# Performance work log

Measured on AMD Instinct MI355X. Metric: run time of the kernel, lower is better.

Reference implementation:

```python
import jax, jax.numpy as jnp
import numpy as np
import math

EMBED = 1024
N_HEAD = 16
T_LEN = 2048
BATCH = 2
MLP_MULT = 4
EPS = 1e-5


def setup_inputs() -> dict:
    key = jax.random.key(0)
    ks = jax.random.split(key, 12)
    d = EMBED
    h = MLP_MULT * d
    s = 0.02
    return {
        "x": jax.random.normal(ks[0], (BATCH, T_LEN, d), dtype=jnp.float32),
        "ln1_scale": jnp.ones((d,), jnp.float32),
        "ln1_shift": jnp.zeros((d,), jnp.float32),
        "w_qkv": jax.random.normal(ks[1], (d, 3 * d), jnp.float32) * s,
        "b_qkv": jnp.zeros((3 * d,), jnp.float32),
        "ln2_scale": jnp.ones((d,), jnp.float32),
        "ln2_shift": jnp.zeros((d,), jnp.float32),
        "w_fc": jax.random.normal(ks[2], (d, h), jnp.float32) * s,
        "b_fc": jnp.zeros((h,), jnp.float32),
        "w_proj": jax.random.normal(ks[3], (h, d), jnp.float32) * s,
        "b_proj": jnp.zeros((d,), jnp.float32),
    }


def _layer_norm(x, scale, shift):
    mu = jnp.mean(x, axis=-1, keepdims=True)
    var = jnp.var(x, axis=-1, keepdims=True)
    return (x - mu) * jax.lax.rsqrt(var + EPS) * scale + shift


def _attention(h, w_qkv, b_qkv):
    B, T, C = h.shape
    hd = C // N_HEAD
    qkv = h @ w_qkv + b_qkv  # [B,T,3C]
    q, k, v = jnp.split(qkv, 3, axis=-1)
    q = q.reshape(B, T, N_HEAD, hd)
    k = k.reshape(B, T, N_HEAD, hd)
    v = v.reshape(B, T, N_HEAD, hd)
    scores = jnp.einsum("bthd,bshd->bhts", q, k) * (1.0 / math.sqrt(hd))
    causal = jnp.tril(jnp.ones((T, T), dtype=bool))
    scores = jnp.where(causal[None, None], scores, -jnp.inf)
    probs = jax.nn.softmax(scores, axis=-1)
    y = jnp.einsum("bhts,bshd->bthd", probs, v)
    return y.reshape(B, T, C)


def reference(x, ln1_scale, ln1_shift, w_qkv, b_qkv, ln2_scale, ln2_shift,
              w_fc, b_fc, w_proj, b_proj):
    x = x + _attention(_layer_norm(x, ln1_scale, ln1_shift), w_qkv, b_qkv)
    h = _layer_norm(x, ln2_scale, ln2_shift)
    # note: module names it 'gelu' but it's nn.ReLU()
    h = jax.nn.relu(h @ w_fc + b_fc) @ w_proj + b_proj
    return x + h
```

## Files before the change

kernel.cpp:

```cpp
#include <hip/hip_runtime.h>
#include <hip/hip_bf16.h>


typedef __bf16  bf16x8  __attribute__((ext_vector_type(8)));
typedef __bf16  bf16x4  __attribute__((ext_vector_type(4)));
typedef float   floatx4 __attribute__((ext_vector_type(4)));

#define T_LEN 2048
#define EMB   1024
#define NH    16
#define HD    64
#define HID   4096

#define GLOBAL_LOAD_LDS16(gp, lp) \
    __builtin_amdgcn_global_load_lds( \
        (const __attribute__((address_space(1))) void*)(gp), \
        (__attribute__((address_space(3))) void*)(lp), 16, 0, 0)

__global__ void transpose_cast(const float* __restrict__ in,
                               __bf16* __restrict__ out, int R, int C) {
    __shared__ float tile[32][33];
    int bc = blockIdx.x * 32;
    int br = blockIdx.y * 32;
    int tx = threadIdx.x;
    int ty = threadIdx.y;
    for (int i = 0; i < 32; i += 8) {
        tile[ty + i][tx] = in[(size_t)(br + ty + i) * C + bc + tx];
    }
    __syncthreads();
    for (int i = 0; i < 32; i += 8) {
        int c = bc + ty + i, r = br + tx;
        out[(size_t)c * R + r] = (__bf16)tile[tx][ty + i];
    }
}

__global__ __launch_bounds__(256)
void ln_kernel(const float* __restrict__ in, const float* __restrict__ sc,
               const float* __restrict__ sh, __bf16* __restrict__ out) {
    int row = blockIdx.x;
    const float* p = in + (size_t)row * EMB;
    int tid = threadIdx.x;
    int lane = tid & 63, wave = tid >> 6;
    float v[4];
    float s = 0.f, s2 = 0.f;
    for (int j = 0; j < 4; j++) {
        v[j] = p[tid + j * 256];
        s += v[j]; s2 += v[j] * v[j];
    }
    for (int m = 1; m < 64; m <<= 1) {
        s  += __shfl_xor(s, m);
        s2 += __shfl_xor(s2, m);
    }
    __shared__ float ssum[4], ssum2[4];
    if (lane == 0) { ssum[wave] = s; ssum2[wave] = s2; }
    __syncthreads();
    float tot  = ssum[0] + ssum[1] + ssum[2] + ssum[3];
    float tot2 = ssum2[0] + ssum2[1] + ssum2[2] + ssum2[3];
    float mean = tot * (1.f / EMB);
    float var  = tot2 * (1.f / EMB) - mean * mean;
    float rstd = rsqrtf(var + 1e-5f);
    for (int j = 0; j < 4; j++) {
        int c = tid + j * 256;
        out[(size_t)row * EMB + c] = (__bf16)((v[j] - mean) * rstd * sc[c] + sh[c]);
    }
}

__global__ __launch_bounds__(512)
void gemm256(const __bf16* __restrict__ A, const __bf16* __restrict__ Bt,
             const float* __restrict__ bias, const float* __restrict__ res,
             float* __restrict__ outF, __bf16* __restrict__ outB,
             int M, int N, int lda, int KL, int relu, int gx, int gz) {
    __shared__ __align__(16) __bf16 sA[2][256][64];
    __shared__ __align__(16) __bf16 sB[2][256][64];
    const int BUFE = 256 * 64;
    int tid  = threadIdx.x;
    int lane = tid & 63, wave = tid >> 6;
    int quad = lane >> 4, l16 = lane & 15;

    int i  = blockIdx.x;
    int c  = i & 7, m = i >> 3;
    int bx = m % gx;
    int p  = (m / gx) * 8 + c;
    int by = p / gz;
    int bz = p - by * gz;

    int bm = by * 256, bn = bx * 256;
    size_t k0 = (size_t)bz * KL;
    int wm = (wave >> 2) * 128, wn = (wave & 3) * 64;

    floatx4 acc[8][4] = {};

    int srow  = tid >> 3;
    int sslot = (tid & 7) ^ (srow & 7);
    const __bf16* gA = A  + (size_t)(bm + srow) * lda + k0 + sslot * 8;
    const __bf16* gB = Bt + (size_t)(bn + srow) * lda + k0 + sslot * 8;
    __bf16* lA = &sA[0][0][0] + wave * 512;
    __bf16* lB = &sB[0][0][0] + wave * 512;
    const size_t rstep = (size_t)64 * lda;

#define STAGE256(nb, ko) do { \
    GLOBAL_LOAD_LDS16(gA + (ko),             lA + (nb) * BUFE); \
    GLOBAL_LOAD_LDS16(gB + (ko),             lB + (nb) * BUFE); \
    GLOBAL_LOAD_LDS16(gA + (ko) + rstep,     lA + (nb) * BUFE + 4096); \
    GLOBAL_LOAD_LDS16(gB + (ko) + rstep,     lB + (nb) * BUFE + 4096); \
    GLOBAL_LOAD_LDS16(gA + (ko) + 2 * rstep, lA + (nb) * BUFE + 8192); \
    GLOBAL_LOAD_LDS16(gB + (ko) + 2 * rstep, lB + (nb) * BUFE + 8192); \
    GLOBAL_LOAD_LDS16(gA + (ko) + 3 * rstep, lA + (nb) * BUFE + 12288); \
    GLOBAL_LOAD_LDS16(gB + (ko) + 3 * rstep, lB + (nb) * BUFE + 12288); \
} while (0)

    STAGE256(0, (size_t)0);

    int xs0  = ((quad) ^ (l16 & 7)) * 8;
    int xs1  = ((4 + quad) ^ (l16 & 7)) * 8;
    int aoff = (wm + l16) * 64;
    int boff = (wn + l16) * 64;

    const int nt = KL / 64;
    for (int t = 0; t < nt; ++t) {
        const int cur = t & 1;
        __builtin_amdgcn_s_barrier();
        asm volatile("" ::: "memory");
        if (t + 1 < nt) {
            STAGE256(cur ^ 1, (size_t)(t + 1) * 64);
            asm volatile("s_waitcnt vmcnt(8)" ::: "memory");
        } else {
            asm volatile("s_waitcnt vmcnt(0)" ::: "memory");
        }
        __builtin_amdgcn_s_barrier();
        asm volatile("" ::: "memory");
        __builtin_amdgcn_sched_barrier(0);

        const __bf16* sAc = &sA[0][0][0] + cur * BUFE;
        const __bf16* sBc = &sB[0][0][0] + cur * BUFE;

        bf16x8 a0[4][2], a1[4][2], b0[2][2], b1[2][2];

        #pragma unroll
        for (int mi = 0; mi < 4; ++mi) {
            a0[mi][0] = *(const bf16x8*)(sAc + aoff + mi * 1024 + xs0);
            a0[mi][1] = *(const bf16x8*)(sAc + aoff + mi * 1024 + xs1);
        }
        #pragma unroll
        for (int nj = 0; nj < 2; ++nj) {
            b0[nj][0] = *(const bf16x8*)(sBc + boff + nj * 1024 + xs0);
            b0[nj][1] = *(const bf16x8*)(sBc + boff + nj * 1024 + xs1);
        }
        __builtin_amdgcn_s_setprio(1);
        #pragma unroll
        for (int ks = 0; ks < 2; ++ks)
            #pragma unroll
            for (int mi = 0; mi < 4; ++mi)
                #pragma unroll
                for (int nj = 0; nj < 2; ++nj)
                    acc[mi][nj] = __builtin_amdgcn_mfma_f32_16x16x32_bf16(
                        a0[mi][ks], b0[nj][ks], acc[mi][nj], 0, 0, 0);
        __builtin_amdgcn_s_setprio(0);

        #pragma unroll
        for (int nj = 0; nj < 2; ++nj) {
            b1[nj][0] = *(const bf16x8*)(sBc + boff + (2 + nj) * 1024 + xs0);
            b1[nj][1] = *(const bf16x8*)(sBc + boff + (2 + nj) * 1024 + xs1);
        }
        __builtin_amdgcn_s_setprio(1);
        #pragma unroll
        for (int ks = 0; ks < 2; ++ks)
            #pragma unroll
            for (int mi = 0; mi < 4; ++mi)
                #pragma unroll
                for (int nj = 0; nj < 2; ++nj)
                    acc[mi][2 + nj] = __builtin_amdgcn_mfma_f32_16x16x32_bf16(
                        a0[mi][ks], b1[nj][ks], acc[mi][2 + nj], 0, 0, 0);
        __builtin_amdgcn_s_setprio(0);

        #pragma unroll
        for (int mi = 0; mi < 4; ++mi) {
            a1[mi][0] = *(const bf16x8*)(sAc + aoff + (4 + mi) * 1024 + xs0);
            a1[mi][1] = *(const bf16x8*)(sAc + aoff + (4 + mi) * 1024 + xs1);
        }
        __builtin_amdgcn_s_setprio(1);
        #pragma unroll
        for (int ks = 0; ks < 2; ++ks)
            #pragma unroll
            for (int mi = 0; mi < 4; ++mi)
                #pragma unroll
                for (int nj = 0; nj < 2; ++nj)
                    acc[4 + mi][2 + nj] = __builtin_amdgcn_mfma_f32_16x16x32_bf16(
                        a1[mi][ks], b1[nj][ks], acc[4 + mi][2 + nj], 0, 0, 0);
        __builtin_amdgcn_s_setprio(0);

        __builtin_amdgcn_s_setprio(1);
        #pragma unroll
        for (int ks = 0; ks < 2; ++ks)
            #pragma unroll
            for (int mi = 0; mi < 4; ++mi)
                #pragma unroll
                for (int nj = 0; nj < 2; ++nj)
                    acc[4 + mi][nj] = __builtin_amdgcn_mfma_f32_16x16x32_bf16(
                        a1[mi][ks], b0[nj][ks], acc[4 + mi][nj], 0, 0, 0);
        __builtin_amdgcn_s_setprio(0);
    }
#undef STAGE256

    if (bias) {
        #pragma unroll
        for (int mi = 0; mi < 8; ++mi) {
            int row0 = bm + wm + mi * 16 + quad * 4;
            #pragma unroll
            for (int nj = 0; nj < 4; ++nj) {
                int col = bn + wn + nj * 16 + l16;
                float bv = bias[col];
                #pragma unroll
                for (int r = 0; r < 4; ++r) {
                    size_t idx = (size_t)(row0 + r) * N + col;
                    float cc = acc[mi][nj][r] + bv;
                    if (relu) cc = fmaxf(cc, 0.f);
                    if (res)  cc += res[idx];
                    if (outF) outF[idx] = cc;
                    if (outB) outB[idx] = (__bf16)cc;
                }
            }
        }
    } else {
        __bf16* po = outB + (size_t)bz * M * N;
        #pragma unroll
        for (int mi = 0; mi < 8; ++mi) {
            int row0 = bm + wm + mi * 16 + quad * 4;
            #pragma unroll
            for (int nj = 0; nj < 4; ++nj) {
                int col = bn + wn + nj * 16 + l16;
                #pragma unroll
                for (int r = 0; r < 4; ++r)
                    po[(size_t)(row0 + r) * N + col] = (__bf16)acc[mi][nj][r];
            }
        }
    }
}

__global__ __launch_bounds__(256)
void reduce_proj(const __bf16* __restrict__ pbuf, const float* __restrict__ x2,
                 const float* __restrict__ bias, float* __restrict__ out) {
    const size_t MN = (size_t)4096 * 1024;
    size_t i = (size_t)blockIdx.x * 256 + threadIdx.x;
    float4 r = ((const float4*)x2)[i];
    float4 bb = ((const float4*)bias)[i & 255];
    float acc0 = r.x + bb.x, acc1 = r.y + bb.y;
    float acc2 = r.z + bb.z, acc3 = r.w + bb.w;
    for (int k = 0; k < 4; k++) {
        bf16x4 pv = *(const bf16x4*)&pbuf[k * MN + i * 4];
        acc0 += (float)pv[0]; acc1 += (float)pv[1];
        acc2 += (float)pv[2]; acc3 += (float)pv[3];
    }
    float4 o = {acc0, acc1, acc2, acc3};
    ((float4*)out)[i] = o;
}

__global__ __launch_bounds__(256)
void gemm_bt_n64(const __bf16* __restrict__ A, const __bf16* __restrict__ Bt,
                 const float* __restrict__ bias, const float* __restrict__ res,
                 float* __restrict__ outF, __bf16* __restrict__ outB,
                 int M, int N, int K, int relu) {
    __shared__ __align__(16) __bf16 sA[128][40];
    __shared__ __align__(16) __bf16 sB[64][40];
    int tid  = threadIdx.x;
    int lane = tid & 63, wave = tid >> 6;
    int quad = lane >> 4, l16 = lane & 15;
    int bm = blockIdx.y * 128, bn = blockIdx.x * 64;
    int wm = (wave & 1) * 64, wn = (wave >> 1) * 32;
    floatx4 acc[4][2] = {};

    int srow = tid >> 2;
    int scol = (tid & 3) * 8;
    const __bf16* gA = &A[(size_t)(bm + srow) * K + scol];
    const __bf16* gB = &Bt[(size_t)(bn + srow) * K + scol];

    uint4 ra0 = *(const uint4*)gA;
    uint4 ra1 = *(const uint4*)(gA + (size_t)64 * K);
    uint4 rb0 = *(const uint4*)gB;

    for (int kk = 0; kk < K; kk += 32) {
        __syncthreads();
        *(uint4*)&sA[srow][scol]      = ra0;
        *(uint4*)&sA[srow + 64][scol] = ra1;
        *(uint4*)&sB[srow][scol]      = rb0;
        __syncthreads();
        {
            int kn = (kk + 32 < K) ? kk + 32 : kk;
            ra0 = *(const uint4*)(gA + kn);
            ra1 = *(const uint4*)(gA + kn + (size_t)64 * K);
            rb0 = *(const uint4*)(gB + kn);
        }
        bf16x8 af[4], bfr[2];
        for (int i = 0; i < 4; i++)
            af[i] = *(const bf16x8*)&sA[wm + i * 16 + l16][quad * 8];
        for (int j = 0; j < 2; j++)
            bfr[j] = *(const bf16x8*)&sB[wn + j * 16 + l16][quad * 8];
        for (int i = 0; i < 4; i++)
            for (int j = 0; j < 2; j++)
                acc[i][j] = __builtin_amdgcn_mfma_f32_16x16x32_bf16(
                    af[i], bfr[j], acc[i][j], 0, 0, 0);
    }

    for (int i = 0; i < 4; i++) {
        int row0 = bm + wm + i * 16 + quad * 4;
        for (int j = 0; j < 2; j++) {
            int col = bn + wn + j * 16 + l16;
            float bv = bias[col];
            for (int r = 0; r < 4; r++) {
                size_t idx = (size_t)(row0 + r) * N + col;
                float c = acc[i][j][r] + bv;
                if (relu) c = fmaxf(c, 0.f);
                if (res)  c += res[idx];
                if (outF) outF[idx] = c;
                if (outB) outB[idx] = (__bf16)c;
            }
        }
    }
}

__global__ __launch_bounds__(512)
void attn_kernel(const __bf16* __restrict__ qkv, const float* __restrict__ x,
                 float* __restrict__ x2) {
    __shared__ __align__(16) __bf16 sK[2][64][72];
    __shared__ __align__(16) __bf16 sVt[2][64][72];
    __shared__ __align__(16) __bf16 sP[8][16][72];
    const int tid  = threadIdx.x;
    const int lane = tid & 63, wave = tid >> 6;
    const int quad = lane >> 4, l16 = lane & 15;

    int i = blockIdx.x;
    int c = i & 7, m = i >> 3;
    const int bh   = (m & 3) * 8 + c;
    const int qt_h = 31 - (m >> 2);
    const int h    = bh & (NH - 1);
    const int b    = bh >> 4;
    const size_t rowbase = (size_t)b * T_LEN;

    const int g  = wave >> 2;
    const int wg = wave & 3;
    const int qt = g ? (31 - qt_h) : qt_h;
    const int qrow = qt * 64 + wg * 16;
    const int dt   = qt;

    const float kQScale = 0.125f * 1.44269504088896f;
    bf16x8 ones;
    for (int j = 0; j < 8; j++) ones[j] = (__bf16)1.0f;

    const int key0 = tid >> 3, m8 = tid & 7;
    const __bf16* kp0 = qkv + (rowbase + key0) * 3072 + h * HD + m8 * 8 + 1024;
    const int pc0 = ((key0 >> 3) ^ m8) * 8 + (key0 & 7);

    bf16x8 qf[2];
    for (int ks = 0; ks < 2; ks++) {
        bf16x8 raw = *(const bf16x8*)&qkv[(rowbase + qrow + l16) * 3072
                                          + h * HD + ks * 32 + quad * 8];
        for (int j = 0; j < 8; j++)
            qf[ks][j] = (__bf16)((float)raw[j] * kQScale);
    }

    floatx4 o[4] = {}, ol = {};

    const int ntiles = qt_h + 1;
    const size_t TSTEP = (size_t)64 * 3072;

    uint4 kr0 = *(const uint4*)kp0;
    uint4 vr0 = *(const uint4*)(kp0 + 1024);
    {
        *(uint4*)&sK[0][key0][m8 * 8] = kr0;
        bf16x8 v0 = *(bf16x8*)&vr0;
        for (int j = 0; j < 8; j++) sVt[0][m8 * 8 + j][pc0] = v0[j];
    }
    kr0 = *(const uint4*)(kp0 + TSTEP);
    vr0 = *(const uint4*)(kp0 + TSTEP + 1024);
    __syncthreads();

    for (int kt = 0; kt < ntiles; kt++) {
        const int cur = kt & 1, nxt = cur ^ 1;
        if (kt + 1 < ntiles) {
            *(uint4*)&sK[nxt][key0][m8 * 8] = kr0;
            bf16x8 v0 = *(bf16x8*)&vr0;
            for (int j = 0; j < 8; j++) sVt[nxt][m8 * 8 + j][pc0] = v0[j];
            size_t offn = (size_t)((kt + 2 < ntiles) ? kt + 2 : kt + 1) * TSTEP;
            kr0 = *(const uint4*)(kp0 + offn);
            vr0 = *(const uint4*)(kp0 + offn + 1024);
        }

        if (kt <= dt) {
            floatx4 s_acc[4] = {};
            for (int jt = 0; jt < 4; jt++)
                for (int ks = 0; ks < 2; ks++) {
                    bf16x8 kf = *(const bf16x8*)&sK[cur][jt * 16 + l16]
                                                  [ks * 32 + quad * 8];
                    s_acc[jt] = __builtin_amdgcn_mfma_f32_16x16x32_bf16(
                        qf[ks], kf, s_acc[jt], 0, 0, 0);
                }

            if (kt == dt) {
                const int tq0 = qrow + quad * 4;
                const int k0 = kt * 64;
                for (int jt = 0; jt < 4; jt++) {
                    int key = k0 + jt * 16 + l16;
                    for (int r = 0; r < 4; r++) {
                        float sv = (key <= tq0 + r) ? s_acc[jt][r] : -1e30f;
                        float pv = __builtin_amdgcn_exp2f(fminf(sv, 30.f));
                        sP[wave][quad * 4 + r][jt * 16 + l16] = (__bf16)pv;
                    }
                }
            } else {
                for (int jt = 0; jt < 4; jt++)
                    for (int r = 0; r < 4; r++) {
                        float pv = __builtin_amdgcn_exp2f(fminf(s_acc[jt][r], 30.f));
                        sP[wave][quad * 4 + r][jt * 16 + l16] = (__bf16)pv;
                    }
            }

            for (int kp = 0; kp < 2; kp++) {
                bf16x8 pf = *(const bf16x8*)&sP[wave][l16][kp * 32 + quad * 8];
                ol = __builtin_amdgcn_mfma_f32_16x16x32_bf16(pf, ones, ol, 0, 0, 0);
                for (int jt2 = 0; jt2 < 4; jt2++) {
                    int d = jt2 * 16 + l16;
                    int pg = (kp * 4 + quad) ^ (d >> 3);
                    bf16x8 vf = *(const bf16x8*)&sVt[cur][d][pg * 8];
                    o[jt2] = __builtin_amdgcn_mfma_f32_16x16x32_bf16(
                        pf, vf, o[jt2], 0, 0, 0);
                }
            }
        }
        __syncthreads();
    }

    float inv[4];
    for (int r = 0; r < 4; r++) inv[r] = __builtin_amdgcn_rcpf(ol[r]);
    for (int jt2 = 0; jt2 < 4; jt2++) {
        for (int r = 0; r < 4; r++) {
            int tq  = qrow + quad * 4 + r;
            int col = h * HD + jt2 * 16 + l16;
            size_t gi = (rowbase + tq) * EMB + col;
            x2[gi] = x[gi] + o[jt2][r] * inv[r];
        }
    }
}

extern "C" void kernel_launch(void* const* d_in, const int* in_sizes, int n_in,
                              void* d_out, int out_size, void* d_ws, size_t ws_size,
                              hipStream_t stream) {
    const float* x      = (const float*)d_in[0];
    const float* ln1_s  = (const float*)d_in[1];
    const float* ln1_b  = (const float*)d_in[2];
    const float* w_qkv  = (const float*)d_in[3];
    const float* b_qkv  = (const float*)d_in[4];
    const float* ln2_s  = (const float*)d_in[5];
    const float* ln2_b  = (const float*)d_in[6];
    const float* w_fc   = (const float*)d_in[7];
    const float* b_fc   = (const float*)d_in[8];
    const float* w_proj = (const float*)d_in[9];
    const float* b_proj = (const float*)d_in[10];
    float* out = (float*)d_out;

    const int M = 2 * T_LEN;
    char* ws = (char*)d_ws;
    size_t off = 0;
    auto alloc = [&](size_t bytes) {
        void* p = ws + off; off += (bytes + 255) & ~(size_t)255; return p;
    };
    __bf16* wpj_t  = (__bf16*)alloc((size_t)1024 * 4096 * 2);
    float*  x2     = (float*) alloc((size_t)M * 1024 * 4);
    __bf16* hfc    = (__bf16*)alloc((size_t)M * 4096 * 2);
    size_t mark = off;
    __bf16* wqkv_t = (__bf16*)alloc((size_t)3072 * 1024 * 2);
    __bf16* wfc_t  = (__bf16*)alloc((size_t)4096 * 1024 * 2);
    __bf16* h1     = (__bf16*)alloc((size_t)M * 1024 * 2);
    __bf16* h2     = (__bf16*)alloc((size_t)M * 1024 * 2);
    __bf16* qkvb   = (__bf16*)alloc((size_t)M * 3072 * 2);
    __bf16* pbuf = (__bf16*)(ws + mark);
    size_t need = mark + (size_t)4 * M * 1024 * 2;
    bool can_split = ws_size >= need;

    dim3 tb(32, 8);
    transpose_cast<<<dim3(3072 / 32, 1024 / 32), tb, 0, stream>>>(w_qkv, wqkv_t, 1024, 3072);
    transpose_cast<<<dim3(4096 / 32, 1024 / 32), tb, 0, stream>>>(w_fc,  wfc_t,  1024, 4096);
    transpose_cast<<<dim3(1024 / 32, 4096 / 32), tb, 0, stream>>>(w_proj, wpj_t, 4096, 1024);

    ln_kernel<<<M, 256, 0, stream>>>(x, ln1_s, ln1_b, h1);

    gemm256<<<192, 512, 0, stream>>>(
        h1, wqkv_t, b_qkv, nullptr, nullptr, qkvb, M, 3072, 1024, 1024, 0,
        12, 1);

    attn_kernel<<<512, 512, 0, stream>>>(qkvb, x, x2);

    ln_kernel<<<M, 256, 0, stream>>>(x2, ln2_s, ln2_b, h2);

    gemm256<<<256, 512, 0, stream>>>(
        h2, wfc_t, b_fc, nullptr, nullptr, hfc, M, 4096, 1024, 1024, 1,
        16, 1);

    if (can_split) {
        gemm256<<<256, 512, 0, stream>>>(
            hfc, wpj_t, nullptr, nullptr, nullptr, pbuf, M, 1024, 4096, 1024, 0,
            4, 4);
        reduce_proj<<<(M * 1024 / 4) / 256, 256, 0, stream>>>(
            pbuf, x2, b_proj, out);
    } else {
        gemm_bt_n64<<<dim3(1024 / 64, M / 128), 256, 0, stream>>>(
            hfc, wpj_t, b_proj, x2, out, nullptr, M, 1024, 4096, 0);
    }
}
```

Measured before the change: 302.2 us.

## Process 32 query rows per wave in attention to reuse K/V fragments

```diff
diff --git a/kernel.cpp b/kernel.cpp
--- a/kernel.cpp
+++ b/kernel.cpp
@@ -318,12 +318,12 @@
     }
 }
 
-__global__ __launch_bounds__(512)
+__global__ __launch_bounds__(256)
 void attn_kernel(const __bf16* __restrict__ qkv, const float* __restrict__ x,
                  float* __restrict__ x2) {
     __shared__ __align__(16) __bf16 sK[2][64][72];
     __shared__ __align__(16) __bf16 sVt[2][64][72];
-    __shared__ __align__(16) __bf16 sP[8][16][72];
+    __shared__ __align__(16) __bf16 sP[4][32][72];
     const int tid  = threadIdx.x;
     const int lane = tid & 63, wave = tid >> 6;
     const int quad = lane >> 4, l16 = lane & 15;
@@ -331,112 +331,158 @@
     int i = blockIdx.x;
     int c = i & 7, m = i >> 3;
     const int bh   = (m & 3) * 8 + c;
-    const int qt_h = 31 - (m >> 2);
+    const int pair = m >> 2;
+    const int qt_h = 31 - pair;
     const int h    = bh & (NH - 1);
     const int b    = bh >> 4;
     const size_t rowbase = (size_t)b * T_LEN;
 
-    const int g  = wave >> 2;
-    const int wg = wave & 3;
-    const int qt = g ? (31 - qt_h) : qt_h;
-    const int qrow = qt * 64 + wg * 16;
-    const int dt   = qt;
+    const int g  = wave >> 1;
+    const int s  = wave & 1;
+    const int qt = g ? pair : qt_h;
+    const int qrow0 = qt * 64 + s * 32;
+    const int dt    = qt;
 
     const float kQScale = 0.125f * 1.44269504088896f;
     bf16x8 ones;
     for (int j = 0; j < 8; j++) ones[j] = (__bf16)1.0f;
 
-    const int key0 = tid >> 3, m8 = tid & 7;
-    const __bf16* kp0 = qkv + (rowbase + key0) * 3072 + h * HD + m8 * 8 + 1024;
-    const int pc0 = ((key0 >> 3) ^ m8) * 8 + (key0 & 7);
-
-    bf16x8 qf[2];
-    for (int ks = 0; ks < 2; ks++) {
-        bf16x8 raw = *(const bf16x8*)&qkv[(rowbase + qrow + l16) * 3072
-                                          + h * HD + ks * 32 + quad * 8];
-        for (int j = 0; j < 8; j++)
-            qf[ks][j] = (__bf16)((float)raw[j] * kQScale);
-    }
-
-    floatx4 o[4] = {}, ol = {};
+    const int key0 = tid >> 2, m4 = tid & 3;
+    const __bf16* kp0 = qkv + (rowbase + key0) * 3072 + h * HD + m4 * 16 + 1024;
+    const int pca = ((key0 >> 3) ^ (2 * m4)) * 8 + (key0 & 7);
+    const int pcb = ((key0 >> 3) ^ (2 * m4 + 1)) * 8 + (key0 & 7);
+
+    bf16x8 qf[2][2];
+    #pragma unroll
+    for (int qi = 0; qi < 2; qi++)
+        #pragma unroll
+        for (int ks = 0; ks < 2; ks++) {
+            bf16x8 raw = *(const bf16x8*)&qkv[(rowbase + qrow0 + qi * 16 + l16)
+                                              * 3072 + h * HD + ks * 32 + quad * 8];
+            for (int j = 0; j < 8; j++)
+                qf[qi][ks][j] = (__bf16)((float)raw[j] * kQScale);
+        }
+
+    floatx4 o[2][4] = {}, ol[2] = {};
 
     const int ntiles = qt_h + 1;
     const size_t TSTEP = (size_t)64 * 3072;
 
-    uint4 kr0 = *(const uint4*)kp0;
-    uint4 vr0 = *(const uint4*)(kp0 + 1024);
+    uint4 ka = *(const uint4*)kp0;
+    uint4 kb = *(const uint4*)(kp0 + 8);
+    uint4 va = *(const uint4*)(kp0 + 1024);
+    uint4 vb = *(const uint4*)(kp0 + 1032);
     {
-        *(uint4*)&sK[0][key0][m8 * 8] = kr0;
-        bf16x8 v0 = *(bf16x8*)&vr0;
-        for (int j = 0; j < 8; j++) sVt[0][m8 * 8 + j][pc0] = v0[j];
-    }
-    kr0 = *(const uint4*)(kp0 + TSTEP);
-    vr0 = *(const uint4*)(kp0 + TSTEP + 1024);
+        *(uint4*)&sK[0][key0][m4 * 16]     = ka;
+        *(uint4*)&sK[0][key0][m4 * 16 + 8] = kb;
+        bf16x8 v0 = *(bf16x8*)&va, v1 = *(bf16x8*)&vb;
+        for (int j = 0; j < 8; j++) sVt[0][(2 * m4) * 8 + j][pca]     = v0[j];
+        for (int j = 0; j < 8; j++) sVt[0][(2 * m4 + 1) * 8 + j][pcb] = v1[j];
+    }
+    ka = *(const uint4*)(kp0 + TSTEP);
+    kb = *(const uint4*)(kp0 + TSTEP + 8);
+    va = *(const uint4*)(kp0 + TSTEP + 1024);
+    vb = *(const uint4*)(kp0 + TSTEP + 1032);
     __syncthreads();
 
     for (int kt = 0; kt < ntiles; kt++) {
         const int cur = kt & 1, nxt = cur ^ 1;
         if (kt + 1 < ntiles) {
-            *(uint4*)&sK[nxt][key0][m8 * 8] = kr0;
-            bf16x8 v0 = *(bf16x8*)&vr0;
-            for (int j = 0; j < 8; j++) sVt[nxt][m8 * 8 + j][pc0] = v0[j];
+            *(uint4*)&sK[nxt][key0][m4 * 16]     = ka;
+            *(uint4*)&sK[nxt][key0][m4 * 16 + 8] = kb;
+            bf16x8 v0 = *(bf16x8*)&va, v1 = *(bf16x8*)&vb;
+            for (int j = 0; j < 8; j++) sVt[nxt][(2 * m4) * 8 + j][pca]     = v0[j];
+            for (int j = 0; j < 8; j++) sVt[nxt][(2 * m4 + 1) * 8 + j][pcb] = v1[j];
             size_t offn = (size_t)((kt + 2 < ntiles) ? kt + 2 : kt + 1) * TSTEP;
-            kr0 = *(const uint4*)(kp0 + offn);
-            vr0 = *(const uint4*)(kp0 + offn + 1024);
+            ka = *(const uint4*)(kp0 + offn);
+            kb = *(const uint4*)(kp0 + offn + 8);
+            va = *(const uint4*)(kp0 + offn + 1024);
+            vb = *(const uint4*)(kp0 + offn + 1032);
         }
 
         if (kt <= dt) {
-            floatx4 s_acc[4] = {};
+            floatx4 s_acc[2][4] = {};
+            #pragma unroll
             for (int jt = 0; jt < 4; jt++)
+                #pragma unroll
                 for (int ks = 0; ks < 2; ks++) {
                     bf16x8 kf = *(const bf16x8*)&sK[cur][jt * 16 + l16]
                                                   [ks * 32 + quad * 8];
-                    s_acc[jt] = __builtin_amdgcn_mfma_f32_16x16x32_bf16(
-                        qf[ks], kf, s_acc[jt], 0, 0, 0);
+                    #pragma unroll
+                    for (int qi = 0; qi < 2; qi++)
+                        s_acc[qi][jt] = __builtin_amdgcn_mfma_f32_16x16x32_bf16(
+                            qf[qi][ks], kf, s_acc[qi][jt], 0, 0, 0);
                 }
 
             if (kt == dt) {
-                const int tq0 = qrow + quad * 4;
                 const int k0 = kt * 64;
-                for (int jt = 0; jt < 4; jt++) {
-                    int key = k0 + jt * 16 + l16;
-                    for (int r = 0; r < 4; r++) {
-                        float sv = (key <= tq0 + r) ? s_acc[jt][r] : -1e30f;
-                        float pv = __builtin_amdgcn_exp2f(fminf(sv, 30.f));
-                        sP[wave][quad * 4 + r][jt * 16 + l16] = (__bf16)pv;
+                #pragma unroll
+                for (int qi = 0; qi < 2; qi++) {
+                    const int tq0 = qrow0 + qi * 16 + quad * 4;
+                    #pragma unroll
+                    for (int jt = 0; jt < 4; jt++) {
+                        int key = k0 + jt * 16 + l16;
+                        #pragma unroll
+                        for (int r = 0; r < 4; r++) {
+                            float sv = (key <= tq0 + r) ? s_acc[qi][jt][r] : -1e30f;
+                            float pv = __builtin_amdgcn_exp2f(fminf(sv, 30.f));
+                            sP[wave][qi * 16 + quad * 4 + r][jt * 16 + l16]
+                                = (__bf16)pv;
+                        }
                     }
                 }
             } else {
-                for (int jt = 0; jt < 4; jt++)
-                    for (int r = 0; r < 4; r++) {
-                        float pv = __builtin_amdgcn_exp2f(fminf(s_acc[jt][r], 30.f));
-                        sP[wave][quad * 4 + r][jt * 16 + l16] = (__bf16)pv;
-                    }
+                #pragma unroll
+                for (int qi = 0; qi < 2; qi++)
+                    #pragma unroll
+                    for (int jt = 0; jt < 4; jt++)
+                        #pragma unroll
+                        for (int r = 0; r < 4; r++) {
+                            float pv = __builtin_amdgcn_exp2f(
+                                fminf(s_acc[qi][jt][r], 30.f));
+                            sP[wave][qi * 16 + quad * 4 + r][jt * 16 + l16]
+                                = (__bf16)pv;
+                        }
             }
 
+            #pragma unroll
             for (int kp = 0; kp < 2; kp++) {
-                bf16x8 pf = *(const bf16x8*)&sP[wave][l16][kp * 32 + quad * 8];
-                ol = __builtin_amdgcn_mfma_f32_16x16x32_bf16(pf, ones, ol, 0, 0, 0);
+                bf16x8 pf[2];
+                #pragma unroll
+                for (int qi = 0; qi < 2; qi++) {
+                    pf[qi] = *(const bf16x8*)&sP[wave][qi * 16 + l16]
+                                                [kp * 32 + quad * 8];
+                    ol[qi] = __builtin_amdgcn_mfma_f32_16x16x32_bf16(
+                        pf[qi], ones, ol[qi], 0, 0, 0);
+                }
+                #pragma unroll
                 for (int jt2 = 0; jt2 < 4; jt2++) {
                     int d = jt2 * 16 + l16;
                     int pg = (kp * 4 + quad) ^ (d >> 3);
                     bf16x8 vf = *(const bf16x8*)&sVt[cur][d][pg * 8];
-                    o[jt2] = __builtin_amdgcn_mfma_f32_16x16x32_bf16(
-                        pf, vf, o[jt2], 0, 0, 0);
+                    #pragma unroll
+                    for (int qi = 0; qi < 2; qi++)
+                        o[qi][jt2] = __builtin_amdgcn_mfma_f32_16x16x32_bf16(
+                            pf[qi], vf, o[qi][jt2], 0, 0, 0);
                 }
             }
         }
         __syncthreads();
     }
 
-    float inv[4];
-    for (int r = 0; r < 4; r++) inv[r] = __builtin_amdgcn_rcpf(ol[r]);
-    for (int jt2 = 0; jt2 < 4; jt2++) {
-        for (int r = 0; r < 4; r++) {
-            int tq  = qrow + quad * 4 + r;
-            int col = h * HD + jt2 * 16 + l16;
-            size_t gi = (rowbase + tq) * EMB + col;
-            x2[gi] = x[gi] + o[jt2][r] * inv[r];
+    #pragma unroll
+    for (int qi = 0; qi < 2; qi++) {
+        float inv[4];
+        for (int r = 0; r < 4; r++) inv[r] = __builtin_amdgcn_rcpf(ol[qi][r]);
+        #pragma unroll
+        for (int jt2 = 0; jt2 < 4; jt2++) {
+            #pragma unroll
+            for (int r = 0; r < 4; r++) {
+                int tq  = qrow0 + qi * 16 + quad * 4 + r;
+                int col = h * HD + jt2 * 16 + l16;
+                size_t gi = (rowbase + tq) * EMB + col;
+                x2[gi] = x[gi] + o[qi][jt2][r] * inv[r];
+            }
         }
     }
 }
@@ -487,7 +533,7 @@
         h1, wqkv_t, b_qkv, nullptr, nullptr, qkvb, M, 3072, 1024, 1024, 0,
         12, 1);
 
-    attn_kernel<<<512, 512, 0, stream>>>(qkvb, x, x2);
+    attn_kernel<<<512, 256, 0, stream>>>(qkvb, x, x2);
 
     ln_kernel<<<M, 256, 0, stream>>>(x2, ln2_s, ln2_b, h2);
 
```

Result: slower. 316.9 us (+4.9%).
